# Kernel tuning notes

Measured on AMD Instinct MI355X. Metric: run time of the kernel, lower is better.

The kernel has to match this reference:

```python
import jax, jax.numpy as jnp
import numpy as np

B, S, E, H = 4, 1024, 1024, 16
D = E // H          # head_dim = 64
ROT = 32            # rotary dims (first ROT channels of each head)


def _rope(x, freqs):
    # x: [B, H, S, D]; freqs: [1, 1, S, ROT]
    r = freqs.shape[-1]
    xl, xr = x[..., :r], x[..., r:]
    half = r // 2
    rot = jnp.concatenate([-xl[..., half:], xl[..., :half]], axis=-1)  # rotate_half
    xl = xl * jnp.cos(freqs) + rot * jnp.sin(freqs)
    return jnp.concatenate([xl, xr], axis=-1)


def setup_inputs() -> dict:
    key = jax.random.key(0)
    ks = jax.random.split(key, 7)
    std = 0.02
    return {
        "hidden_states": jax.random.normal(ks[0], (B, S, E), jnp.float32),
        "rotary_pos_emb": jax.random.normal(ks[1], (1, S, ROT), jnp.float32),
        "q_w": jax.random.normal(ks[2], (E, E), jnp.float32) * std,
        "k_w": jax.random.normal(ks[3], (E, E), jnp.float32) * std,
        "v_w": jax.random.normal(ks[4], (E, E), jnp.float32) * std,
        "o_w": jax.random.normal(ks[5], (E, E), jnp.float32) * std,
        "o_b": jnp.zeros((E,), jnp.float32),
    }


def reference(hidden_states, rotary_pos_emb, q_w, k_w, v_w, o_w, o_b):
    bsz, tgt_len, embed_dim = hidden_states.shape
    scale = D ** -0.5

    def shape(t):  # [B, S, E] -> [B, H, S, D]
        return t.reshape(bsz, tgt_len, H, D).transpose(0, 2, 1, 3)

    q = shape(hidden_states @ q_w.T * scale)
    k = shape(hidden_states @ k_w.T)
    v = shape(hidden_states @ v_w.T)

    freqs = rotary_pos_emb[:, None, :, :]  # [1, 1, S, ROT]
    q = _rope(q, freqs)
    k = _rope(k, freqs)
    v = _rope(v, freqs)

    attn = jnp.einsum("bhqd,bhkd->bhqk", q, k)
    causal = jnp.tril(jnp.ones((tgt_len, tgt_len), bool))
    attn = jnp.where(causal, attn, jnp.finfo(attn.dtype).min)
    attn = jax.nn.softmax(attn, axis=-1)

    out = jnp.einsum("bhqk,bhkd->bhqd", attn, v)
    out = out.transpose(0, 2, 1, 3).reshape(bsz, tgt_len, embed_dim)
    return out @ o_w.T + o_b
```

## Files before the change

kernel.cpp:

```cpp
#include <hip/hip_runtime.h>
#include <hip/hip_bf16.h>

typedef __bf16 bf16;
typedef __attribute__((ext_vector_type(2))) __bf16 bf16x2;
typedef __attribute__((ext_vector_type(4))) __bf16 bf16x4;
typedef __attribute__((ext_vector_type(8))) __bf16 bf16x8;
typedef __attribute__((ext_vector_type(4))) float f32x4;

#define NB 4
#define NS 1024
#define NE 1024
#define NH 16
#define ND 64
#define NROT 32
#define NM (NB*NS)

__device__ __forceinline__ void gload_lds16(const bf16* g, void* l) {
  __builtin_amdgcn_global_load_lds(
      (const __attribute__((address_space(1))) unsigned int*)g,
      (__attribute__((address_space(3))) unsigned int*)l,
      16, 0, 0);
}

struct PrepArgs {
  const float* w0; const float* w1; const float* w2; const float* w3;
  bf16* b0; bf16* b1; bf16* b2; bf16* b3;
  const float* hs; bf16* hb;
  const float* rot; float* ct; float* st;
};
__global__ void k_prep(PrepArgs a) {
  const int y = blockIdx.y;
  const int i = blockIdx.x * 256 + threadIdx.x;
  if (y < 4) {
    const float* s = (y == 0) ? a.w0 : (y == 1) ? a.w1 : (y == 2) ? a.w2 : a.w3;
    bf16* d = (y == 0) ? a.b0 : (y == 1) ? a.b1 : (y == 2) ? a.b2 : a.b3;
    float4 v = reinterpret_cast<const float4*>(s)[i];
    bf16x4 o = { (bf16)v.x, (bf16)v.y, (bf16)v.z, (bf16)v.w };
    *reinterpret_cast<bf16x4*>(d + (size_t)i * 4) = o;
  } else if (y < 8) {
    size_t off = (size_t)(y - 4) * (NM * NE / 16);
    float4 v = reinterpret_cast<const float4*>(a.hs)[off + i];
    bf16x4 o = { (bf16)v.x, (bf16)v.y, (bf16)v.z, (bf16)v.w };
    *reinterpret_cast<bf16x4*>(a.hb + (off + i) * 4) = o;
  } else {
    if (i < NS * NROT) {
      float v = a.rot[i];
      a.ct[i] = cosf(v);
      a.st[i] = sinf(v);
    }
  }
}

template<bool SWAP>
__device__ __forceinline__ void gemm_core256(
    const bf16* __restrict__ A, const bf16* __restrict__ W,
    bf16* lA, bf16* lB, int m0, int n0, f32x4 (&acc)[32])
{
  const int tid = threadIdx.x;
  const int wave = tid >> 6, lane = tid & 63;
  const int wm = wave >> 2, wn = wave & 3;
  const int fr = lane & 15, kg = lane >> 4;
  const int lrow8 = lane >> 3, lslot = lane & 7;

  auto stageH = [&](int kt, int c, int h) {
    const bf16* src = (h < 2) ? A : W;
    bf16* dst = (h < 2) ? lA : lB;
    const int base0 = (h < 2) ? m0 : n0;
    const int hh = h & 1;
#pragma unroll
    for (int i = 0; i < 2; ++i) {
      int chunk = hh * 16 + i * 8 + wave;
      int row = (chunk << 3) + lrow8;
      int slot = lslot ^ (row & 7);
      gload_lds16(src + (size_t)(base0 + row) * NE + kt + slot * 8,
                  (char*)dst + c * 32768 + chunk * 1024);
    }
  };

#pragma unroll
  for (int h = 0; h < 4; ++h) stageH(0, 0, h);
  asm volatile("s_waitcnt vmcnt(0)\n\ts_barrier" ::: "memory");

  constexpr int NT = NE / 64;
  bf16x8 bfrag[4][2];

  for (int t = 0; t < NT; ++t) {
    const int c = t & 1;
    const char* cA = (const char*)lA + c * 32768;
    const char* cB = (const char*)lB + c * 32768;

#pragma unroll
    for (int q = 0; q < 4; ++q) {
      if (t + 1 < NT) {
        if (q == 0) { stageH((t + 1) * 64, c ^ 1, 0); stageH((t + 1) * 64, c ^ 1, 1); }
        else if (q < 3) stageH((t + 1) * 64, c ^ 1, q + 1);
      }

      if (q == 0) {
        if (t > 0) {
          if (t + 1 < NT)
            asm volatile("s_waitcnt vmcnt(4)\n\ts_barrier" ::: "memory");
          else
            asm volatile("s_waitcnt vmcnt(0)\n\ts_barrier" ::: "memory");
        }
#pragma unroll
        for (int j = 0; j < 4; ++j) {
          int rb = wn * 64 + j * 16 + fr;
#pragma unroll
          for (int kk = 0; kk < 2; ++kk)
            bfrag[j][kk] = *reinterpret_cast<const bf16x8*>(
                cB + rb * 128 + (((kg + 4 * kk) ^ (rb & 7)) << 4));
        }
      }

      bf16x8 af[2][2];
#pragma unroll
      for (int u = 0; u < 2; ++u) {
        int ra = wm * 128 + (2 * q + u) * 16 + fr;
#pragma unroll
        for (int kk = 0; kk < 2; ++kk)
          af[u][kk] = *reinterpret_cast<const bf16x8*>(
              cA + ra * 128 + (((kg + 4 * kk) ^ (ra & 7)) << 4));
      }

      __builtin_amdgcn_sched_barrier(0);
      __builtin_amdgcn_s_setprio(1);
#pragma unroll
      for (int kk = 0; kk < 2; ++kk)
#pragma unroll
        for (int u = 0; u < 2; ++u)
#pragma unroll
          for (int j = 0; j < 4; ++j) {
            const int i = 2 * q + u;
            if constexpr (SWAP)
              acc[j * 8 + i] = __builtin_amdgcn_mfma_f32_16x16x32_bf16(
                  bfrag[j][kk], af[u][kk], acc[j * 8 + i], 0, 0, 0);
            else
              acc[i * 4 + j] = __builtin_amdgcn_mfma_f32_16x16x32_bf16(
                  af[u][kk], bfrag[j][kk], acc[i * 4 + j], 0, 0, 0);
          }
      __builtin_amdgcn_s_setprio(0);
      __builtin_amdgcn_sched_barrier(0);
    }

    asm volatile("s_waitcnt lgkmcnt(0)\n\ts_barrier" ::: "memory");
  }
}

__global__ __launch_bounds__(512) void k_proj(
    const bf16* __restrict__ A, const bf16* __restrict__ Wq, const bf16* __restrict__ Wk,
    const bf16* __restrict__ Wv, bf16* __restrict__ Oq, bf16* __restrict__ Ok,
    bf16* __restrict__ vt, const float* __restrict__ ct, const float* __restrict__ st)
{
  __shared__ bf16 lA[2 * 256 * 64];
  __shared__ bf16 lB[2 * 256 * 64];
  const int z = blockIdx.z;
  const int m0 = blockIdx.x * 256, n0 = blockIdx.y * 256;
  const int tid = threadIdx.x;
  const int wave = tid >> 6, lane = tid & 63;
  const int wm = wave >> 2, wn = wave & 3;
  const int fr = lane & 15, kg = lane >> 4;

  f32x4 acc[32] = {};

  if (z == 2) {
    gemm_core256<true>(A, Wv, lA, lB, m0, n0, acc);

    const int b = m0 >> 10;
    const int h = (n0 + wn * 64) >> 6;
    bf16* vtb = vt + ((size_t)(b * 16 + h)) * ND * NS;
#pragma unroll
    for (int i = 0; i < 8; ++i) {
      int sl = (m0 & (NS - 1)) + wm * 128 + i * 16 + fr;
#pragma unroll
      for (int r = 0; r < 4; ++r) {
        int dbase = kg * 4 + r;
        float x0 = acc[0 * 8 + i][r];
        float x1 = acc[1 * 8 + i][r];
        float c0 = ct[sl * NROT + dbase],      sn0 = st[sl * NROT + dbase];
        float c1 = ct[sl * NROT + 16 + dbase], sn1 = st[sl * NROT + 16 + dbase];
        float y0 = x0 * c0 - x1 * sn0;
        float y1 = x1 * c1 + x0 * sn1;
        vtb[(size_t)(dbase)      * NS + sl] = (bf16)y0;
        vtb[(size_t)(16 + dbase) * NS + sl] = (bf16)y1;
        vtb[(size_t)(32 + dbase) * NS + sl] = (bf16)acc[2 * 8 + i][r];
        vtb[(size_t)(48 + dbase) * NS + sl] = (bf16)acc[3 * 8 + i][r];
      }
    }
  } else {
    const bf16* W = (z == 0) ? Wq : Wk;
    bf16* Og = (z == 0) ? Oq : Ok;
    const float scale = (z == 0) ? 0.125f * 1.44269504f : 1.0f;

    gemm_core256<false>(A, W, lA, lB, m0, n0, acc);

#pragma unroll
    for (int i = 0; i < 8; ++i) {
      int rowbase = m0 + wm * 128 + i * 16 + kg * 4;
#pragma unroll
      for (int r = 0; r < 4; ++r) {
        int gm = rowbase + r;
        int s = gm & (NS - 1);
        float x0 = acc[i * 4 + 0][r] * scale;
        float x1 = acc[i * 4 + 1][r] * scale;
        float c0 = ct[s * NROT + fr],      sn0 = st[s * NROT + fr];
        float c1 = ct[s * NROT + 16 + fr], sn1 = st[s * NROT + 16 + fr];
        float y0 = x0 * c0 - x1 * sn0;
        float y1 = x1 * c1 + x0 * sn1;
        size_t rb = (size_t)gm * NE + n0 + wn * 64;
        Og[rb + 0 * 16 + fr] = (bf16)y0;
        Og[rb + 1 * 16 + fr] = (bf16)y1;
        Og[rb + 2 * 16 + fr] = (bf16)(acc[i * 4 + 2][r] * scale);
        Og[rb + 3 * 16 + fr] = (bf16)(acc[i * 4 + 3][r] * scale);
      }
    }
  }
}

__global__ __launch_bounds__(256) void k_gemm_o(
    const bf16* __restrict__ A, const bf16* __restrict__ W, float* __restrict__ Og,
    const float* __restrict__ bias)
{
  __shared__ bf16 lA[64 * 64];
  __shared__ bf16 lB[128 * 64];
  const int m0 = blockIdx.x * 64, n0 = blockIdx.y * 128;
  const int tid = threadIdx.x;
  const int wave = tid >> 6, lane = tid & 63;
  const int wm = wave >> 1, wn = wave & 1;
  const int fr = lane & 15, kg = lane >> 4;
  const int lrow8 = lane >> 3, lslot = lane & 7;

  f32x4 acc[2][4] = {};

  for (int kt = 0; kt < NE; kt += 64) {
#pragma unroll
    for (int i = 0; i < 2; ++i) {
      int chunk = i * 4 + wave;
      int row = (chunk << 3) + lrow8;
      int slot = lslot ^ (row & 7);
      gload_lds16(A + (size_t)(m0 + row) * NE + kt + slot * 8, (char*)lA + chunk * 1024);
    }
#pragma unroll
    for (int i = 0; i < 4; ++i) {
      int chunk = i * 4 + wave;
      int row = (chunk << 3) + lrow8;
      int slot = lslot ^ (row & 7);
      gload_lds16(W + (size_t)(n0 + row) * NE + kt + slot * 8, (char*)lB + chunk * 1024);
    }
    __syncthreads();
#pragma unroll
    for (int kk = 0; kk < 2; ++kk) {
      bf16x8 af[2], bfr[4];
#pragma unroll
      for (int i = 0; i < 2; ++i) {
        int ra = wm * 32 + i * 16 + fr;
        af[i] = *reinterpret_cast<const bf16x8*>(lA + ra * 64 + (((kg + 4 * kk) ^ (ra & 7)) << 3));
      }
#pragma unroll
      for (int j = 0; j < 4; ++j) {
        int rb = wn * 64 + j * 16 + fr;
        bfr[j] = *reinterpret_cast<const bf16x8*>(lB + rb * 64 + (((kg + 4 * kk) ^ (rb & 7)) << 3));
      }
#pragma unroll
      for (int i = 0; i < 2; ++i)
#pragma unroll
        for (int j = 0; j < 4; ++j)
          acc[i][j] = __builtin_amdgcn_mfma_f32_16x16x32_bf16(af[i], bfr[j], acc[i][j], 0, 0, 0);
    }
    __syncthreads();
  }

#pragma unroll
  for (int i = 0; i < 2; ++i)
#pragma unroll
    for (int j = 0; j < 4; ++j) {
      int gc = n0 + wn * 64 + j * 16 + fr;
      float bv = bias[gc];
#pragma unroll
      for (int r = 0; r < 4; ++r) {
        int gm = m0 + wm * 32 + i * 16 + kg * 4 + r;
        Og[(size_t)gm * NE + gc] = acc[i][j][r] + bv;
      }
    }
}

__global__ __launch_bounds__(256) void k_attn(
    const bf16* __restrict__ Q, const bf16* __restrict__ K,
    const bf16* __restrict__ VT, bf16* __restrict__ O)
{
  __shared__ bf16 lK[2][64 * 64];
  __shared__ bf16 lVT[2][64 * 64];
  __shared__ bf16 lP[4][16 * 68];
  const int tid = threadIdx.x;
  const int wave = tid >> 6, lane = tid & 63;
  const int fr = lane & 15, kg = lane >> 4;

  const int qt = 15 - (blockIdx.y >> 3);
  const int bh = blockIdx.x | ((blockIdx.y & 7) << 3);
  const int b = bh >> 4, h = bh & 15;
  const int nt = qt + 1;
  const bf16* Qb  = Q + (size_t)b * NS * NE + h * 64;
  const bf16* Kb  = K + (size_t)b * NS * NE + h * 64;
  const bf16* VTb = VT + (size_t)bh * ND * NS;
  bf16* Ob = O + (size_t)b * NS * NE + h * 64;

  const int qrow0 = qt * 64 + wave * 16;

  bf16x8 qf[2];
#pragma unroll
  for (int kk = 0; kk < 2; ++kk)
    qf[kk] = *reinterpret_cast<const bf16x8*>(
        Qb + (size_t)(qrow0 + fr) * NE + kk * 32 + kg * 8);

  const int srow = lane >> 3;
  const int sslot = (lane & 7) ^ srow;
  const int r0 = wave * 8 + srow;
  const int r1 = (wave + 4) * 8 + srow;
  const bf16* kA0 = Kb + (size_t)r0 * NE + sslot * 8;
  const bf16* kA1 = Kb + (size_t)r1 * NE + sslot * 8;
  const bf16* vA0 = VTb + (size_t)r0 * NS + sslot * 8;
  const bf16* vA1 = VTb + (size_t)r1 * NS + sslot * 8;
  char* ldsKa[2] = { (char*)lK[0] + wave * 1024, (char*)lK[1] + wave * 1024 };
  char* ldsKb[2] = { (char*)lK[0] + (wave + 4) * 1024, (char*)lK[1] + (wave + 4) * 1024 };
  char* ldsVa[2] = { (char*)lVT[0] + wave * 1024, (char*)lVT[1] + wave * 1024 };
  char* ldsVb[2] = { (char*)lVT[0] + (wave + 4) * 1024, (char*)lVT[1] + (wave + 4) * 1024 };

  float m_ = -3.0e38f, l_ = 0.f;
  f32x4 oacc[4] = {};

  gload_lds16(kA0, ldsKa[0]);
  gload_lds16(kA1, ldsKb[0]);
  gload_lds16(vA0, ldsVa[0]);
  gload_lds16(vA1, ldsVb[0]);
  __syncthreads();

  for (int t = 0; t < nt; ++t) {
    const int c = t & 1;
    if (t + 1 < nt) {
      gload_lds16(kA0 + (size_t)(t + 1) * 64 * NE, ldsKa[c ^ 1]);
      gload_lds16(kA1 + (size_t)(t + 1) * 64 * NE, ldsKb[c ^ 1]);
      gload_lds16(vA0 + (t + 1) * 64, ldsVa[c ^ 1]);
      gload_lds16(vA1 + (t + 1) * 64, ldsVb[c ^ 1]);
    }

    const bf16* lKc = lK[c];
    f32x4 sacc[4] = {};
    __builtin_amdgcn_s_setprio(1);
#pragma unroll
    for (int kk = 0; kk < 2; ++kk)
#pragma unroll
      for (int j = 0; j < 4; ++j) {
        int rc = j * 16 + fr;
        bf16x8 kf = *reinterpret_cast<const bf16x8*>(
            lKc + rc * 64 + (((kg + 4 * kk) ^ (rc & 7)) << 3));
        sacc[j] = __builtin_amdgcn_mfma_f32_16x16x32_bf16(kf, qf[kk], sacc[j], 0, 0, 0);
      }
    __builtin_amdgcn_s_setprio(0);

    if (t == qt) {
      const int ql = wave * 16 + fr;
#pragma unroll
      for (int j = 0; j < 4; ++j)
#pragma unroll
        for (int r = 0; r < 4; ++r)
          if (16 * j + 4 * kg + r > ql) sacc[j][r] = -3.0e38f;
    }

    float m4 = fmaxf(fmaxf(fmaxf(sacc[0][0], sacc[0][1]), fmaxf(sacc[0][2], sacc[0][3])),
                     fmaxf(fmaxf(sacc[1][0], sacc[1][1]), fmaxf(sacc[1][2], sacc[1][3])));
    m4 = fmaxf(m4, fmaxf(fmaxf(fmaxf(sacc[2][0], sacc[2][1]), fmaxf(sacc[2][2], sacc[2][3])),
                         fmaxf(fmaxf(sacc[3][0], sacc[3][1]), fmaxf(sacc[3][2], sacc[3][3]))));
    m4 = fmaxf(m4, __shfl_xor(m4, 16));
    m4 = fmaxf(m4, __shfl_xor(m4, 32));

    if (!__all(m4 - m_ <= 8.0f)) {
      float nm = fmaxf(m_, m4);
      float corr = exp2f(m_ - nm);
      m_ = nm;
      l_ *= corr;
#pragma unroll
      for (int r = 0; r < 4; ++r) {
        float cr = __shfl(corr, kg * 4 + r);
#pragma unroll
        for (int df = 0; df < 4; ++df) oacc[df][r] *= cr;
      }
    }

    float ps = 0.f;
#pragma unroll
    for (int j = 0; j < 4; ++j) {
      float p0 = exp2f(sacc[j][0] - m_);
      float p1 = exp2f(sacc[j][1] - m_);
      float p2 = exp2f(sacc[j][2] - m_);
      float p3 = exp2f(sacc[j][3] - m_);
      ps += (p0 + p1) + (p2 + p3);
      bf16x4 pp = { (bf16)p0, (bf16)p1, (bf16)p2, (bf16)p3 };
      *reinterpret_cast<bf16x4*>(&lP[wave][fr * 68 + j * 16 + kg * 4]) = pp;
    }
    ps += __shfl_xor(ps, 16);
    ps += __shfl_xor(ps, 32);
    l_ += ps;

    const bf16* lVc = lVT[c];
    __builtin_amdgcn_s_setprio(1);
#pragma unroll
    for (int ks = 0; ks < 2; ++ks) {
      bf16x8 pf = *reinterpret_cast<const bf16x8*>(&lP[wave][fr * 68 + ks * 32 + kg * 8]);
#pragma unroll
      for (int df = 0; df < 4; ++df) {
        int d = df * 16 + fr;
        bf16x8 vf = *reinterpret_cast<const bf16x8*>(
            lVc + d * 64 + (((kg + 4 * ks) ^ (d & 7)) << 3));
        oacc[df] = __builtin_amdgcn_mfma_f32_16x16x32_bf16(pf, vf, oacc[df], 0, 0, 0);
      }
    }
    __builtin_amdgcn_s_setprio(0);

    if (t + 1 < nt)
      asm volatile("s_waitcnt vmcnt(0)\n\ts_barrier" ::: "memory");
  }

  float linv[4];
#pragma unroll
  for (int r = 0; r < 4; ++r) linv[r] = 1.0f / __shfl(l_, kg * 4 + r);
#pragma unroll
  for (int df = 0; df < 4; ++df)
#pragma unroll
    for (int r = 0; r < 4; ++r)
      Ob[(size_t)(qrow0 + kg * 4 + r) * NE + df * 16 + fr] = (bf16)(oacc[df][r] * linv[r]);
}

extern "C" void kernel_launch(void* const* d_in, const int* in_sizes, int n_in,
                              void* d_out, int out_size, void* d_ws, size_t ws_size,
                              hipStream_t stream) {
  const float* hs  = (const float*)d_in[0];
  const float* rot = (const float*)d_in[1];
  const float* qw  = (const float*)d_in[2];
  const float* kw  = (const float*)d_in[3];
  const float* vw  = (const float*)d_in[4];
  const float* ow  = (const float*)d_in[5];
  const float* obb = (const float*)d_in[6];
  float* out = (float*)d_out;

  char* ws = (char*)d_ws;
  size_t off = 0;
  bf16* hb  = (bf16*)(ws + off); off += (size_t)NM * NE * 2;
  bf16* wqb = (bf16*)(ws + off); off += (size_t)NE * NE * 2;
  bf16* wkb = (bf16*)(ws + off); off += (size_t)NE * NE * 2;
  bf16* wvb = (bf16*)(ws + off); off += (size_t)NE * NE * 2;
  bf16* wob = (bf16*)(ws + off); off += (size_t)NE * NE * 2;
  bf16* qb  = (bf16*)(ws + off); off += (size_t)NM * NE * 2;
  bf16* kb  = (bf16*)(ws + off); off += (size_t)NM * NE * 2;
  bf16* vt  = (bf16*)(ws + off); off += (size_t)NM * NE * 2;
  float* ct = (float*)(ws + off); off += (size_t)NS * NROT * 4;
  float* st = (float*)(ws + off); off += (size_t)NS * NROT * 4;
  bf16* aob = hb;

  PrepArgs pa = { qw, kw, vw, ow, wqb, wkb, wvb, wob, hs, hb, rot, ct, st };
  k_prep<<<dim3(NE * NE / 4 / 256, 9), dim3(256), 0, stream>>>(pa);

  k_proj<<<dim3(NM / 256, NE / 256, 3), dim3(512), 0, stream>>>(
      hb, wqb, wkb, wvb, qb, kb, vt, ct, st);

  k_attn<<<dim3(8, 128), dim3(256), 0, stream>>>(qb, kb, vt, aob);

  k_gemm_o<<<dim3(NM / 64, NE / 128), dim3(256), 0, stream>>>(aob, wob, out, obb);

  (void)in_sizes; (void)n_in; (void)out_size; (void)ws_size;
}
```

Before: 95.44 us.

## Fuse Q/K/V projections into one block sharing the staged activation tile

The QKV projection kernel no longer launches a separate 256x256 tile per weight matrix. Each block now computes a 128x128 output tile for all three of Q, K and V, so one staged activation tile in LDS feeds three weight tiles. This aims to cut redundant global and LDS loads of the activations and to give a 256-block grid instead of 192 larger blocks. In exchange the per-wave output tile shrinks, which lowers MFMA work per LDS fragment load. The RoPE epilogue now branches on whether the wave's 32 columns fall in the rotary half of a head.

Result: no change. 96.37 us (+1.0%).

```diff
diff --git a/kernel.cpp b/kernel.cpp
--- a/kernel.cpp
+++ b/kernel.cpp
@@ -51,49 +51,54 @@
   }
 }
 
-template<bool SWAP>
-__device__ __forceinline__ void gemm_core256(
-    const bf16* __restrict__ A, const bf16* __restrict__ W,
-    bf16* lA, bf16* lB, int m0, int n0, f32x4 (&acc)[32])
+__global__ __launch_bounds__(512) void k_proj(
+    const bf16* __restrict__ A, const bf16* __restrict__ Wq, const bf16* __restrict__ Wk,
+    const bf16* __restrict__ Wv, bf16* __restrict__ Oq, bf16* __restrict__ Ok,
+    bf16* __restrict__ vt, const float* __restrict__ ct, const float* __restrict__ st)
 {
+  __shared__ bf16 lA[2 * 128 * 64];
+  __shared__ bf16 lW[3][2 * 128 * 64];
+  const int m0 = blockIdx.x * 128, n0 = blockIdx.y * 128;
   const int tid = threadIdx.x;
   const int wave = tid >> 6, lane = tid & 63;
   const int wm = wave >> 2, wn = wave & 3;
   const int fr = lane & 15, kg = lane >> 4;
   const int lrow8 = lane >> 3, lslot = lane & 7;
 
-  auto stageH = [&](int kt, int c, int h) {
-    const bf16* src = (h < 2) ? A : W;
-    bf16* dst = (h < 2) ? lA : lB;
-    const int base0 = (h < 2) ? m0 : n0;
-    const int hh = h & 1;
+  auto stageG = [&](int kt, int c, int g) {
+    const bf16* src = (g == 0) ? A : (g == 1) ? Wq : (g == 2) ? Wk : Wv;
+    bf16* dst = (g == 0) ? lA : lW[g - 1];
+    const int base0 = (g == 0) ? m0 : n0;
 #pragma unroll
     for (int i = 0; i < 2; ++i) {
-      int chunk = hh * 16 + i * 8 + wave;
+      int chunk = wave * 2 + i;
       int row = (chunk << 3) + lrow8;
       int slot = lslot ^ (row & 7);
       gload_lds16(src + (size_t)(base0 + row) * NE + kt + slot * 8,
-                  (char*)dst + c * 32768 + chunk * 1024);
+                  (char*)dst + c * 16384 + chunk * 1024);
     }
   };
 
 #pragma unroll
-  for (int h = 0; h < 4; ++h) stageH(0, 0, h);
+  for (int g = 0; g < 4; ++g) stageG(0, 0, g);
   asm volatile("s_waitcnt vmcnt(0)\n\ts_barrier" ::: "memory");
 
   constexpr int NT = NE / 64;
-  bf16x8 bfrag[4][2];
+  f32x4 aq[4][2] = {}, ak[4][2] = {}, av[2][4] = {};
+  bf16x8 bq[2][2], bk[2][2], bv[2][2];
 
   for (int t = 0; t < NT; ++t) {
     const int c = t & 1;
-    const char* cA = (const char*)lA + c * 32768;
-    const char* cB = (const char*)lB + c * 32768;
+    const bf16* cA = lA + c * 8192;
+    const bf16* cQ = lW[0] + c * 8192;
+    const bf16* cK = lW[1] + c * 8192;
+    const bf16* cV = lW[2] + c * 8192;
 
 #pragma unroll
     for (int q = 0; q < 4; ++q) {
       if (t + 1 < NT) {
-        if (q == 0) { stageH((t + 1) * 64, c ^ 1, 0); stageH((t + 1) * 64, c ^ 1, 1); }
-        else if (q < 3) stageH((t + 1) * 64, c ^ 1, q + 1);
+        if (q == 0) { stageG((t + 1) * 64, c ^ 1, 0); stageG((t + 1) * 64, c ^ 1, 1); }
+        else if (q < 3) stageG((t + 1) * 64, c ^ 1, q + 1);
       }
 
       if (q == 0) {
@@ -104,23 +109,24 @@
             asm volatile("s_waitcnt vmcnt(0)\n\ts_barrier" ::: "memory");
         }
 #pragma unroll
-        for (int j = 0; j < 4; ++j) {
-          int rb = wn * 64 + j * 16 + fr;
-#pragma unroll
-          for (int kk = 0; kk < 2; ++kk)
-            bfrag[j][kk] = *reinterpret_cast<const bf16x8*>(
-                cB + rb * 128 + (((kg + 4 * kk) ^ (rb & 7)) << 4));
+        for (int j = 0; j < 2; ++j) {
+          int rb = wn * 32 + j * 16 + fr;
+          int off0 = rb * 64 + (((kg + 0) ^ (rb & 7)) << 3);
+          int off1 = rb * 64 + (((kg + 4) ^ (rb & 7)) << 3);
+          bq[j][0] = *reinterpret_cast<const bf16x8*>(cQ + off0);
+          bq[j][1] = *reinterpret_cast<const bf16x8*>(cQ + off1);
+          bk[j][0] = *reinterpret_cast<const bf16x8*>(cK + off0);
+          bk[j][1] = *reinterpret_cast<const bf16x8*>(cK + off1);
+          bv[j][0] = *reinterpret_cast<const bf16x8*>(cV + off0);
+          bv[j][1] = *reinterpret_cast<const bf16x8*>(cV + off1);
         }
       }
 
-      bf16x8 af[2][2];
-#pragma unroll
-      for (int u = 0; u < 2; ++u) {
-        int ra = wm * 128 + (2 * q + u) * 16 + fr;
-#pragma unroll
-        for (int kk = 0; kk < 2; ++kk)
-          af[u][kk] = *reinterpret_cast<const bf16x8*>(
-              cA + ra * 128 + (((kg + 4 * kk) ^ (ra & 7)) << 4));
+      bf16x8 af[2];
+      {
+        int ra = wm * 64 + q * 16 + fr;
+        af[0] = *reinterpret_cast<const bf16x8*>(cA + ra * 64 + (((kg + 0) ^ (ra & 7)) << 3));
+        af[1] = *reinterpret_cast<const bf16x8*>(cA + ra * 64 + (((kg + 4) ^ (ra & 7)) << 3));
       }
 
       __builtin_amdgcn_sched_barrier(0);
@@ -128,90 +134,68 @@
 #pragma unroll
       for (int kk = 0; kk < 2; ++kk)
 #pragma unroll
-        for (int u = 0; u < 2; ++u)
-#pragma unroll
-          for (int j = 0; j < 4; ++j) {
-            const int i = 2 * q + u;
-            if constexpr (SWAP)
-              acc[j * 8 + i] = __builtin_amdgcn_mfma_f32_16x16x32_bf16(
-                  bfrag[j][kk], af[u][kk], acc[j * 8 + i], 0, 0, 0);
-            else
-              acc[i * 4 + j] = __builtin_amdgcn_mfma_f32_16x16x32_bf16(
-                  af[u][kk], bfrag[j][kk], acc[i * 4 + j], 0, 0, 0);
-          }
+        for (int j = 0; j < 2; ++j) {
+          aq[q][j] = __builtin_amdgcn_mfma_f32_16x16x32_bf16(af[kk], bq[j][kk], aq[q][j], 0, 0, 0);
+          ak[q][j] = __builtin_amdgcn_mfma_f32_16x16x32_bf16(af[kk], bk[j][kk], ak[q][j], 0, 0, 0);
+          av[j][q] = __builtin_amdgcn_mfma_f32_16x16x32_bf16(bv[j][kk], af[kk], av[j][q], 0, 0, 0);
+        }
       __builtin_amdgcn_s_setprio(0);
       __builtin_amdgcn_sched_barrier(0);
     }
 
     asm volatile("s_waitcnt lgkmcnt(0)\n\ts_barrier" ::: "memory");
   }
-}
-
-__global__ __launch_bounds__(512) void k_proj(
-    const bf16* __restrict__ A, const bf16* __restrict__ Wq, const bf16* __restrict__ Wk,
-    const bf16* __restrict__ Wv, bf16* __restrict__ Oq, bf16* __restrict__ Ok,
-    bf16* __restrict__ vt, const float* __restrict__ ct, const float* __restrict__ st)
-{
-  __shared__ bf16 lA[2 * 256 * 64];
-  __shared__ bf16 lB[2 * 256 * 64];
-  const int z = blockIdx.z;
-  const int m0 = blockIdx.x * 256, n0 = blockIdx.y * 256;
-  const int tid = threadIdx.x;
-  const int wave = tid >> 6, lane = tid & 63;
-  const int wm = wave >> 2, wn = wave & 3;
-  const int fr = lane & 15, kg = lane >> 4;
-
-  f32x4 acc[32] = {};
-
-  if (z == 2) {
-    gemm_core256<true>(A, Wv, lA, lB, m0, n0, acc);
-
+
+  const int nb = n0 + wn * 32;
+  const bool ropeHalf = ((nb & 63) == 0);
+  const float qscale = 0.125f * 1.44269504f;
+
+#pragma unroll
+  for (int p = 0; p < 4; ++p)
+#pragma unroll
+    for (int r = 0; r < 4; ++r) {
+      int gm = m0 + wm * 64 + p * 16 + kg * 4 + r;
+      int s = gm & (NS - 1);
+      size_t rb = (size_t)gm * NE + nb;
+      float q0v = aq[p][0][r] * qscale, q1v = aq[p][1][r] * qscale;
+      float k0v = ak[p][0][r],          k1v = ak[p][1][r];
+      if (ropeHalf) {
+        float c0 = ct[s * NROT + fr],      sn0 = st[s * NROT + fr];
+        float c1 = ct[s * NROT + 16 + fr], sn1 = st[s * NROT + 16 + fr];
+        Oq[rb + fr]      = (bf16)(q0v * c0 - q1v * sn0);
+        Oq[rb + 16 + fr] = (bf16)(q1v * c1 + q0v * sn1);
+        Ok[rb + fr]      = (bf16)(k0v * c0 - k1v * sn0);
+        Ok[rb + 16 + fr] = (bf16)(k1v * c1 + k0v * sn1);
+      } else {
+        Oq[rb + fr]      = (bf16)q0v;
+        Oq[rb + 16 + fr] = (bf16)q1v;
+        Ok[rb + fr]      = (bf16)k0v;
+        Ok[rb + 16 + fr] = (bf16)k1v;
+      }
+    }
+
+  {
     const int b = m0 >> 10;
-    const int h = (n0 + wn * 64) >> 6;
+    const int h = nb >> 6;
+    const int eb = nb & 63;
     bf16* vtb = vt + ((size_t)(b * 16 + h)) * ND * NS;
 #pragma unroll
-    for (int i = 0; i < 8; ++i) {
-      int sl = (m0 & (NS - 1)) + wm * 128 + i * 16 + fr;
+    for (int i = 0; i < 4; ++i) {
+      int sl = (m0 & (NS - 1)) + wm * 64 + i * 16 + fr;
 #pragma unroll
       for (int r = 0; r < 4; ++r) {
         int dbase = kg * 4 + r;
-        float x0 = acc[0 * 8 + i][r];
-        float x1 = acc[1 * 8 + i][r];
-        float c0 = ct[sl * NROT + dbase],      sn0 = st[sl * NROT + dbase];
-        float c1 = ct[sl * NROT + 16 + dbase], sn1 = st[sl * NROT + 16 + dbase];
-        float y0 = x0 * c0 - x1 * sn0;
-        float y1 = x1 * c1 + x0 * sn1;
-        vtb[(size_t)(dbase)      * NS + sl] = (bf16)y0;
-        vtb[(size_t)(16 + dbase) * NS + sl] = (bf16)y1;
-        vtb[(size_t)(32 + dbase) * NS + sl] = (bf16)acc[2 * 8 + i][r];
-        vtb[(size_t)(48 + dbase) * NS + sl] = (bf16)acc[3 * 8 + i][r];
-      }
-    }
-  } else {
-    const bf16* W = (z == 0) ? Wq : Wk;
-    bf16* Og = (z == 0) ? Oq : Ok;
-    const float scale = (z == 0) ? 0.125f * 1.44269504f : 1.0f;
-
-    gemm_core256<false>(A, W, lA, lB, m0, n0, acc);
-
-#pragma unroll
-    for (int i = 0; i < 8; ++i) {
-      int rowbase = m0 + wm * 128 + i * 16 + kg * 4;
-#pragma unroll
-      for (int r = 0; r < 4; ++r) {
-        int gm = rowbase + r;
-        int s = gm & (NS - 1);
-        float x0 = acc[i * 4 + 0][r] * scale;
-        float x1 = acc[i * 4 + 1][r] * scale;
-        float c0 = ct[s * NROT + fr],      sn0 = st[s * NROT + fr];
-        float c1 = ct[s * NROT + 16 + fr], sn1 = st[s * NROT + 16 + fr];
-        float y0 = x0 * c0 - x1 * sn0;
-        float y1 = x1 * c1 + x0 * sn1;
-        size_t rb = (size_t)gm * NE + n0 + wn * 64;
-        Og[rb + 0 * 16 + fr] = (bf16)y0;
-        Og[rb + 1 * 16 + fr] = (bf16)y1;
-        Og[rb + 2 * 16 + fr] = (bf16)(acc[i * 4 + 2][r] * scale);
-        Og[rb + 3 * 16 + fr] = (bf16)(acc[i * 4 + 3][r] * scale);
+        float x0 = av[0][i][r];
+        float x1 = av[1][i][r];
+        if (eb == 0) {
+          float c0 = ct[sl * NROT + dbase],      sn0 = st[sl * NROT + dbase];
+          float c1 = ct[sl * NROT + 16 + dbase], sn1 = st[sl * NROT + 16 + dbase];
+          vtb[(size_t)(dbase)      * NS + sl] = (bf16)(x0 * c0 - x1 * sn0);
+          vtb[(size_t)(16 + dbase) * NS + sl] = (bf16)(x1 * c1 + x0 * sn1);
+        } else {
+          vtb[(size_t)(32 + dbase) * NS + sl] = (bf16)x0;
+          vtb[(size_t)(48 + dbase) * NS + sl] = (bf16)x1;
+        }
       }
     }
   }
@@ -459,7 +443,7 @@
   PrepArgs pa = { qw, kw, vw, ow, wqb, wkb, wvb, wob, hs, hb, rot, ct, st };
   k_prep<<<dim3(NE * NE / 4 / 256, 9), dim3(256), 0, stream>>>(pa);
 
-  k_proj<<<dim3(NM / 256, NE / 256, 3), dim3(512), 0, stream>>>(
+  k_proj<<<dim3(NM / 128, NE / 128), dim3(512), 0, stream>>>(
       hb, wqb, wkb, wvb, qb, kb, vt, ct, st);
 
   k_attn<<<dim3(8, 128), dim3(256), 0, stream>>>(qb, kb, vt, aob);
```
